# Optimization experiments

Measured on AMD Instinct MI355X. Metric: run time of the kernel, lower is better.

## Reference

```python
import jax, jax.numpy as jnp
import numpy as np

N = 100000
E = 3200000
F_IN, F_HID, F_OUT = 512, 16, 40


def setup_inputs() -> dict:
    key = jax.random.key(0)
    k1, k2, k3, k4 = jax.random.split(key, 4)
    x = jax.random.normal(k1, (N, F_IN), dtype=jnp.float32)
    edge_index = jax.random.randint(k2, (2, E), 0, N, dtype=jnp.int64)
    # Glorot-style init for the two GCN layer weights + zero biases
    W1 = jax.random.normal(k3, (F_IN, F_HID), dtype=jnp.float32) / np.sqrt(F_IN)
    b1 = jnp.zeros((F_HID,), dtype=jnp.float32)
    W2 = jax.random.normal(k4, (F_HID, F_OUT), dtype=jnp.float32) / np.sqrt(F_HID)
    b2 = jnp.zeros((F_OUT,), dtype=jnp.float32)
    return {"x": x, "edge_index": edge_index, "W1": W1, "b1": b1, "W2": W2, "b2": b2}


def _gcn_conv(x, src, dst, W, b):
    # x' = D^{-1/2} (A + I) D^{-1/2} (x W) + b   (standard GCNConv with self-loops)
    n = x.shape[0]
    h = x @ W  # [N, F_out] -- transform first (cheap edge traffic)
    deg = jax.ops.segment_sum(jnp.ones_like(dst, dtype=h.dtype), dst, num_segments=n) + 1.0  # +1 self-loop
    dinv = jax.lax.rsqrt(deg)
    msgs = h[src] * (dinv[src] * dinv[dst])[:, None]  # [E, F_out]
    agg = jax.ops.segment_sum(msgs, dst, num_segments=n)
    agg = agg + h * (dinv * dinv)[:, None]  # self-loop contribution
    return agg + b


def reference(x, edge_index, W1, b1, W2, b2):
    src, dst = edge_index[0], edge_index[1]
    h = _gcn_conv(x, src, dst, W1, b1)
    h = jax.nn.relu(h)
    # dropout is identity in eval mode (training=False)
    h = _gcn_conv(h, src, dst, W2, b2)
    return jax.nn.log_softmax(h, axis=1)
```

## Files before the change

### kernel.cpp

```cpp
#include <hip/hip_runtime.h>
#include <hip/hip_fp16.h>
#include <math.h>

#define FIN 512
#define FH 16
#define FOUT 40
#define RANGE 128
#define RSH 7
#define NB_MAX 1024
#define SRC_BITS 17
#define SRC_MASK 0x1FFFF
#define BCHUNK 4096
#define HCHUNK 16384
#define AP 17
#define GCHUNK 4096

__global__ __launch_bounds__(256) void histA_k(const int* __restrict__ dst, int E, int NB,
                                               unsigned* __restrict__ bcnt) {
  __shared__ unsigned h[NB_MAX];
  for (int b = threadIdx.x; b < NB; b += 256) h[b] = 0;
  __syncthreads();
  const int base = blockIdx.x * HCHUNK;
  const int cn = min(HCHUNK, E - base);
  for (int u = threadIdx.x; u < cn; u += 256)
    atomicAdd(&h[((unsigned)dst[base + u]) >> RSH], 1u);
  __syncthreads();
  for (int b = threadIdx.x; b < NB; b += 256) {
    unsigned c = h[b];
    if (c) atomicAdd(&bcnt[b], c);
  }
}

__global__ __launch_bounds__(1024) void scanB_k(const unsigned* __restrict__ bcnt, int NB,
                                                unsigned* __restrict__ boff,
                                                unsigned* __restrict__ bcur) {
  __shared__ unsigned ws[16];
  const int t = threadIdx.x, lane = t & 63, wid = t >> 6;
  unsigned v = (t < NB) ? bcnt[t] : 0;
  unsigned incl = v;
#pragma unroll
  for (int d = 1; d < 64; d <<= 1) {
    unsigned o = __shfl_up(incl, d);
    if (lane >= d) incl += o;
  }
  if (lane == 63) ws[wid] = incl;
  __syncthreads();
  unsigned woff = 0, tot = 0;
#pragma unroll
  for (int w = 0; w < 16; ++w) {
    unsigned s = ws[w];
    if (w < wid) woff += s;
    tot += s;
  }
  unsigned ex = woff + incl - v;
  if (t < NB) { boff[t] = ex; bcur[t] = ex; }
  if (t == 0) boff[NB] = tot;
}

__global__ __launch_bounds__(256) void bin_k(const int* __restrict__ src,
                                             const int* __restrict__ dst, int E, int NB,
                                             unsigned* __restrict__ bcur,
                                             unsigned* __restrict__ bins) {
  __shared__ unsigned hist[NB_MAX];
  __shared__ unsigned excl[NB_MAX];
  __shared__ unsigned gbase[NB_MAX];
  __shared__ unsigned lcur[NB_MAX];
  __shared__ unsigned stage[BCHUNK];
  __shared__ unsigned short sbkt[BCHUNK];
  __shared__ unsigned wtot[4];
  const int t = threadIdx.x, lane = t & 63, wid = t >> 6;
  for (int b = t; b < NB; b += 256) hist[b] = 0;
  __syncthreads();
  const int base = blockIdx.x * BCHUNK;
  const int cn = min(BCHUNK, E - base);
  for (int u = t; u < cn; u += 256)
    atomicAdd(&hist[((unsigned)dst[base + u]) >> RSH], 1u);
  __syncthreads();
  unsigned loc[4], s = 0;
#pragma unroll
  for (int j = 0; j < 4; ++j) {
    int idx = t * 4 + j;
    loc[j] = s;
    s += (idx < NB) ? hist[idx] : 0;
  }
  unsigned incl = s;
#pragma unroll
  for (int d = 1; d < 64; d <<= 1) {
    unsigned o = __shfl_up(incl, d);
    if (lane >= d) incl += o;
  }
  if (lane == 63) wtot[wid] = incl;
  __syncthreads();
  unsigned woff = 0;
  for (int w = 0; w < wid; ++w) woff += wtot[w];
  unsigned tex = woff + incl - s;
#pragma unroll
  for (int j = 0; j < 4; ++j) {
    int idx = t * 4 + j;
    if (idx < NB) excl[idx] = tex + loc[j];
  }
  __syncthreads();
  for (int b = t; b < NB; b += 256) {
    unsigned c = hist[b];
    gbase[b] = c ? atomicAdd(&bcur[b], c) : 0u;
    lcur[b] = excl[b];
  }
  __syncthreads();
  for (int u = t; u < cn; u += 256) {
    int e = base + u;
    unsigned d = (unsigned)dst[e];
    unsigned bkt = d >> RSH;
    unsigned pk = ((unsigned)src[e]) | ((d & (RANGE - 1)) << SRC_BITS);
    unsigned lr = atomicAdd(&lcur[bkt], 1u);
    stage[lr] = pk;
    sbkt[lr] = (unsigned short)bkt;
  }
  __syncthreads();
  for (int u = t; u < cn; u += 256) {
    unsigned bkt = sbkt[u];
    bins[gbase[bkt] + (u - excl[bkt])] = stage[u];
  }
}

__global__ __launch_bounds__(256) void deg_k(const unsigned* __restrict__ boff,
                                             const unsigned* __restrict__ bins, int n,
                                             float* __restrict__ dinv) {
  __shared__ unsigned dh[RANGE];
  const int t = threadIdx.x, b = blockIdx.x;
  if (t < RANGE) dh[t] = 0;
  __syncthreads();
  const unsigned jb = boff[b], je = boff[b + 1];
  for (unsigned j = jb + t; j < je; j += 256) atomicAdd(&dh[bins[j] >> SRC_BITS], 1u);
  __syncthreads();
  const int i = b * RANGE + t;
  if (t < RANGE && i < n) dinv[i] = rsqrtf((float)dh[t] + 1.0f);
}

__global__ __launch_bounds__(256) void gemm1_k(const float* __restrict__ x,
                                               const float* __restrict__ W1,
                                               const float* __restrict__ dinv, int n,
                                               __half* __restrict__ hs1) {
  __shared__ float w1s[FIN * FH];
  for (int idx = threadIdx.x; idx < FIN * FH; idx += 256) w1s[idx] = W1[idx];
  __syncthreads();

  const int row_raw = blockIdx.x * 256 + threadIdx.x;
  const int row = row_raw < n ? row_raw : n - 1;
  const float4* __restrict__ xr = (const float4*)(x + (size_t)row * FIN);

  float4 a0 = {0, 0, 0, 0}, a1 = {0, 0, 0, 0}, a2 = {0, 0, 0, 0}, a3 = {0, 0, 0, 0};

#pragma unroll 2
  for (int it = 0; it < FIN / 4; ++it) {
    float4 xv = xr[it];
    const float* wf = w1s + it * 4 * FH;
#pragma unroll
    for (int j = 0; j < 4; ++j) {
      const float xj = (j == 0) ? xv.x : (j == 1) ? xv.y : (j == 2) ? xv.z : xv.w;
      const float* wj = wf + j * FH;
      float4 w0 = *(const float4*)(wj + 0);
      float4 w1 = *(const float4*)(wj + 4);
      float4 w2 = *(const float4*)(wj + 8);
      float4 w3 = *(const float4*)(wj + 12);
      a0.x += xj * w0.x; a0.y += xj * w0.y; a0.z += xj * w0.z; a0.w += xj * w0.w;
      a1.x += xj * w1.x; a1.y += xj * w1.y; a1.z += xj * w1.z; a1.w += xj * w1.w;
      a2.x += xj * w2.x; a2.y += xj * w2.y; a2.z += xj * w2.z; a2.w += xj * w2.w;
      a3.x += xj * w3.x; a3.y += xj * w3.y; a3.z += xj * w3.z; a3.w += xj * w3.w;
    }
  }

  if (row_raw < n) {
    const float di = dinv[row];
    __half2 hb[8];
    hb[0] = __floats2half2_rn(a0.x * di, a0.y * di);
    hb[1] = __floats2half2_rn(a0.z * di, a0.w * di);
    hb[2] = __floats2half2_rn(a1.x * di, a1.y * di);
    hb[3] = __floats2half2_rn(a1.z * di, a1.w * di);
    hb[4] = __floats2half2_rn(a2.x * di, a2.y * di);
    hb[5] = __floats2half2_rn(a2.z * di, a2.w * di);
    hb[6] = __floats2half2_rn(a3.x * di, a3.y * di);
    hb[7] = __floats2half2_rn(a3.z * di, a3.w * di);
    uint4* o = (uint4*)(hs1 + (size_t)row * FH);
    o[0] = ((const uint4*)hb)[0];
    o[1] = ((const uint4*)hb)[1];
  }
}

__device__ __forceinline__ void accum_row(float* __restrict__ arow, uint4 q0, uint4 q1) {
  float2 f;
  f = __half22float2(*(const __half2*)&q0.x); atomicAdd(arow + 0, f.x);  atomicAdd(arow + 1, f.y);
  f = __half22float2(*(const __half2*)&q0.y); atomicAdd(arow + 2, f.x);  atomicAdd(arow + 3, f.y);
  f = __half22float2(*(const __half2*)&q0.z); atomicAdd(arow + 4, f.x);  atomicAdd(arow + 5, f.y);
  f = __half22float2(*(const __half2*)&q0.w); atomicAdd(arow + 6, f.x);  atomicAdd(arow + 7, f.y);
  f = __half22float2(*(const __half2*)&q1.x); atomicAdd(arow + 8, f.x);  atomicAdd(arow + 9, f.y);
  f = __half22float2(*(const __half2*)&q1.y); atomicAdd(arow + 10, f.x); atomicAdd(arow + 11, f.y);
  f = __half22float2(*(const __half2*)&q1.z); atomicAdd(arow + 12, f.x); atomicAdd(arow + 13, f.y);
  f = __half22float2(*(const __half2*)&q1.w); atomicAdd(arow + 14, f.x); atomicAdd(arow + 15, f.y);
}

__device__ __forceinline__ void edge_phase(const __half* __restrict__ tab,
                                           const unsigned* __restrict__ bins,
                                           unsigned jb, unsigned je, int t,
                                           float* __restrict__ acc) {
  for (unsigned cb = jb; cb < je; cb += GCHUNK) {
    const unsigned j0 = cb + t;
    unsigned pk[8];
    bool val[8];
#pragma unroll
    for (int i = 0; i < 8; ++i) {
      const unsigned j = j0 + i * 512;
      val[i] = (j < je);
      pk[i] = val[i] ? bins[j] : 0u;
    }
    uint4 q0[8], q1[8];
#pragma unroll
    for (int i = 0; i < 8; ++i) {
      const uint4* rp = (const uint4*)(tab + (size_t)(pk[i] & SRC_MASK) * FH);
      q0[i] = rp[0];
      q1[i] = rp[1];
    }
#pragma unroll
    for (int i = 0; i < 8; ++i) {
      if (val[i]) accum_row(acc + (pk[i] >> SRC_BITS) * AP, q0[i], q1[i]);
    }
  }
}

__global__ __launch_bounds__(512, 4) void gather1_k(const __half* __restrict__ hs1,
                                                    const unsigned* __restrict__ boff,
                                                    const unsigned* __restrict__ bins,
                                                    const float* __restrict__ dinv,
                                                    const float* __restrict__ b1, int n,
                                                    __half* __restrict__ rs) {
  __shared__ float acc[RANGE * AP];
  __shared__ float b1s[FH];
  const int t = threadIdx.x, b = blockIdx.x;
  if (t < FH) b1s[t] = b1[t];
  for (int u = t; u < RANGE * AP; u += 512) acc[u] = 0.f;
  __syncthreads();
  const unsigned jb = boff[b], je = boff[b + 1];
  edge_phase(hs1, bins, jb, je, t, acc);
  __syncthreads();
  const int base = b * RANGE;
  {
    const int node = t >> 2, sub = t & 3;
    const int i = base + node;
    if (i < n) {
      const float* arow = acc + node * AP + sub * 4;
      const float a0 = arow[0], a1 = arow[1], a2 = arow[2], a3 = arow[3];
      const __half2* hp = (const __half2*)(hs1 + (size_t)i * FH + sub * 4);
      const float2 h0 = __half22float2(hp[0]);
      const float2 h1 = __half22float2(hp[1]);
      const float d = dinv[i];
      float r0 = (a0 + h0.x) * d + b1s[sub * 4 + 0];
      float r1 = (a1 + h0.y) * d + b1s[sub * 4 + 1];
      float r2 = (a2 + h1.x) * d + b1s[sub * 4 + 2];
      float r3 = (a3 + h1.y) * d + b1s[sub * 4 + 3];
      r0 = fmaxf(r0, 0.f) * d;
      r1 = fmaxf(r1, 0.f) * d;
      r2 = fmaxf(r2, 0.f) * d;
      r3 = fmaxf(r3, 0.f) * d;
      __half2* rp = (__half2*)(rs + (size_t)i * FH + sub * 4);
      rp[0] = __floats2half2_rn(r0, r1);
      rp[1] = __floats2half2_rn(r2, r3);
    }
  }
}

__global__ __launch_bounds__(512, 4) void gather2_k(const __half* __restrict__ rs,
                                                    const unsigned* __restrict__ boff,
                                                    const unsigned* __restrict__ bins,
                                                    const float* __restrict__ dinv,
                                                    const float* __restrict__ W2,
                                                    const float* __restrict__ b2, int n,
                                                    float* __restrict__ out) {
  __shared__ float acc[RANGE * AP];
  __shared__ float w2s[FH * FOUT + FOUT];
  const int t = threadIdx.x, b = blockIdx.x;
  for (int idx = t; idx < FH * FOUT + FOUT; idx += 512)
    w2s[idx] = (idx < FH * FOUT) ? W2[idx] : b2[idx - FH * FOUT];
  for (int u = t; u < RANGE * AP; u += 512) acc[u] = 0.f;
  __syncthreads();
  const unsigned jb = boff[b], je = boff[b + 1];
  edge_phase(rs, bins, jb, je, t, acc);
  __syncthreads();
  const int base = b * RANGE;
  {
    const int node = t >> 2, sub = t & 3;
    const int i = base + node;
    if (i < n) {
      float* arow = acc + node * AP + sub * 4;
      const __half2* rp = (const __half2*)(rs + (size_t)i * FH + sub * 4);
      const float2 r0 = __half22float2(rp[0]);
      const float2 r1 = __half22float2(rp[1]);
      const float d = dinv[i];
      arow[0] = (arow[0] + r0.x) * d;
      arow[1] = (arow[1] + r0.y) * d;
      arow[2] = (arow[2] + r1.x) * d;
      arow[3] = (arow[3] + r1.y) * d;
    }
  }
  __syncthreads();
  const int lane = t & 63, wv = t >> 6;
  for (int nd = wv; nd < RANGE; nd += 8) {
    const int i = base + nd;
    if (i >= n) continue;
    float hv = (lane < FOUT) ? w2s[FH * FOUT + lane] : 0.f;
#pragma unroll
    for (int kk = 0; kk < 16; ++kk) {
      const float a = acc[nd * AP + kk];
      if (lane < FOUT) hv += a * w2s[kk * FOUT + lane];
    }
    float m = (lane < FOUT) ? hv : -INFINITY;
#pragma unroll
    for (int d = 1; d < 64; d <<= 1) m = fmaxf(m, __shfl_xor(m, d));
    float ex = (lane < FOUT) ? expf(hv - m) : 0.f;
#pragma unroll
    for (int d = 1; d < 64; d <<= 1) ex += __shfl_xor(ex, d);
    if (lane < FOUT) out[(size_t)i * FOUT + lane] = hv - m - logf(ex);
  }
}

extern "C" void kernel_launch(void* const* d_in, const int* in_sizes, int n_in,
                              void* d_out, int out_size, void* d_ws, size_t ws_size,
                              hipStream_t stream) {
  const float* x  = (const float*)d_in[0];
  const int*   ei = (const int*)d_in[1];
  const float* W1 = (const float*)d_in[2];
  const float* b1 = (const float*)d_in[3];
  const float* W2 = (const float*)d_in[4];
  const float* b2 = (const float*)d_in[5];
  float* out = (float*)d_out;

  const int n = in_sizes[0] / FIN;
  const int E = in_sizes[1] / 2;
  const int* src = ei;
  const int* dst = ei + E;
  const int NB = (n + RANGE - 1) >> RSH;

  char* ws = (char*)d_ws;
  size_t o = 0;
  auto alloc = [&](size_t bytes) {
    void* p = ws + o;
    o = (o + bytes + 255) & ~(size_t)255;
    return p;
  };
  unsigned* bcnt = (unsigned*)alloc((size_t)(NB + 1) * 4);
  unsigned* boff = (unsigned*)alloc((size_t)(NB + 1) * 4);
  unsigned* bcur = (unsigned*)alloc((size_t)NB * 4);
  float*    dinv = (float*)alloc((size_t)n * 4);
  unsigned* bins = (unsigned*)alloc((size_t)E * 4);
  __half*   hs1  = (__half*)alloc((size_t)n * FH * 2);
  __half*   rsb  = (__half*)alloc((size_t)n * FH * 2);

  hipMemsetAsync(bcnt, 0, (size_t)(NB + 1) * 4, stream);

  histA_k<<<(E + HCHUNK - 1) / HCHUNK, 256, 0, stream>>>(dst, E, NB, bcnt);
  scanB_k<<<1, 1024, 0, stream>>>(bcnt, NB, boff, bcur);
  bin_k<<<(E + BCHUNK - 1) / BCHUNK, 256, 0, stream>>>(src, dst, E, NB, bcur, bins);
  deg_k<<<NB, 256, 0, stream>>>(boff, bins, n, dinv);

  gemm1_k<<<(n + 255) / 256, 256, 0, stream>>>(x, W1, dinv, n, hs1);
  gather1_k<<<NB, 512, 0, stream>>>(hs1, boff, bins, dinv, b1, n, rsb);
  gather2_k<<<NB, 512, 0, stream>>>(rsb, boff, bins, dinv, W2, b2, n, out);
}
```

Measured before the change: 879.4 us.

## Stage gathered feature rows into LDS via direct global-to-LDS loads per wave

Rewrites the edge gather so each wave fetches neighbor feature rows straight into a per-wave LDS staging buffer using global_load_lds with 16-byte transfers. Two lanes now share each edge, each handling half of the 16-wide row, and each wave works through 128 edges per iteration. This replaces the old scheme where one thread per edge held 8 rows in registers, aiming to cut register pressure and issue gathers more efficiently. In exchange it adds 32KB of LDS per block, waits for all loads with a full vmcnt(0) barrier every iteration with no double buffering, and drops the occupancy hint from the launch bounds.

```diff
diff --git a/kernel.cpp b/kernel.cpp
--- a/kernel.cpp
+++ b/kernel.cpp
@@ -13,7 +13,14 @@
 #define BCHUNK 4096
 #define HCHUNK 16384
 #define AP 17
-#define GCHUNK 4096
+#define WED 128
+
+typedef unsigned int u32;
+
+__device__ __forceinline__ void gload_lds16(const void* g, void* l) {
+  __builtin_amdgcn_global_load_lds((const __attribute__((address_space(1))) u32*)g,
+                                   (__attribute__((address_space(3))) u32*)l, 16, 0, 0);
+}
 
 __global__ __launch_bounds__(256) void histA_k(const int* __restrict__ dst, int E, int NB,
                                                unsigned* __restrict__ bcnt) {
@@ -186,60 +193,56 @@
   }
 }
 
-__device__ __forceinline__ void accum_row(float* __restrict__ arow, uint4 q0, uint4 q1) {
-  float2 f;
-  f = __half22float2(*(const __half2*)&q0.x); atomicAdd(arow + 0, f.x);  atomicAdd(arow + 1, f.y);
-  f = __half22float2(*(const __half2*)&q0.y); atomicAdd(arow + 2, f.x);  atomicAdd(arow + 3, f.y);
-  f = __half22float2(*(const __half2*)&q0.z); atomicAdd(arow + 4, f.x);  atomicAdd(arow + 5, f.y);
-  f = __half22float2(*(const __half2*)&q0.w); atomicAdd(arow + 6, f.x);  atomicAdd(arow + 7, f.y);
-  f = __half22float2(*(const __half2*)&q1.x); atomicAdd(arow + 8, f.x);  atomicAdd(arow + 9, f.y);
-  f = __half22float2(*(const __half2*)&q1.y); atomicAdd(arow + 10, f.x); atomicAdd(arow + 11, f.y);
-  f = __half22float2(*(const __half2*)&q1.z); atomicAdd(arow + 12, f.x); atomicAdd(arow + 13, f.y);
-  f = __half22float2(*(const __half2*)&q1.w); atomicAdd(arow + 14, f.x); atomicAdd(arow + 15, f.y);
-}
-
 __device__ __forceinline__ void edge_phase(const __half* __restrict__ tab,
                                            const unsigned* __restrict__ bins,
                                            unsigned jb, unsigned je, int t,
+                                           __half* __restrict__ stage,
                                            float* __restrict__ acc) {
-  for (unsigned cb = jb; cb < je; cb += GCHUNK) {
-    const unsigned j0 = cb + t;
-    unsigned pk[8];
-    bool val[8];
-#pragma unroll
-    for (int i = 0; i < 8; ++i) {
-      const unsigned j = j0 + i * 512;
-      val[i] = (j < je);
-      pk[i] = val[i] ? bins[j] : 0u;
-    }
-    uint4 q0[8], q1[8];
-#pragma unroll
-    for (int i = 0; i < 8; ++i) {
-      const uint4* rp = (const uint4*)(tab + (size_t)(pk[i] & SRC_MASK) * FH);
-      q0[i] = rp[0];
-      q1[i] = rp[1];
-    }
-#pragma unroll
-    for (int i = 0; i < 8; ++i) {
-      if (val[i]) accum_row(acc + (pk[i] >> SRC_BITS) * AP, q0[i], q1[i]);
-    }
-  }
-}
-
-__global__ __launch_bounds__(512, 4) void gather1_k(const __half* __restrict__ hs1,
-                                                    const unsigned* __restrict__ boff,
-                                                    const unsigned* __restrict__ bins,
-                                                    const float* __restrict__ dinv,
-                                                    const float* __restrict__ b1, int n,
-                                                    __half* __restrict__ rs) {
+  const int l = t & 63, wv = t >> 6;
+  __half* swv = stage + wv * (WED * FH);
+  for (unsigned c = jb + (unsigned)wv * WED; c < je; c += 8u * WED) {
+    unsigned pk[4];
+    bool vld[4];
+#pragma unroll
+    for (int r = 0; r < 4; ++r) {
+      const unsigned e = c + r * 32u + (unsigned)(l >> 1);
+      vld[r] = (e < je);
+      pk[r] = bins[vld[r] ? e : (je - 1)];
+      const unsigned row = vld[r] ? (pk[r] & SRC_MASK) : 0u;
+      const __half* g = tab + (size_t)row * FH + (l & 1) * 8;
+      gload_lds16(g, swv + r * 512 + l * 8);
+    }
+    asm volatile("s_waitcnt vmcnt(0)" ::: "memory");
+    __builtin_amdgcn_sched_barrier(0);
+#pragma unroll
+    for (int r = 0; r < 4; ++r) {
+      if (!vld[r]) continue;
+      const uint4 q = *(const uint4*)(swv + r * 512 + l * 8);
+      float* arow = acc + (pk[r] >> SRC_BITS) * AP + (l & 1) * 8;
+      float2 f;
+      f = __half22float2(*(const __half2*)&q.x); atomicAdd(arow + 0, f.x); atomicAdd(arow + 1, f.y);
+      f = __half22float2(*(const __half2*)&q.y); atomicAdd(arow + 2, f.x); atomicAdd(arow + 3, f.y);
+      f = __half22float2(*(const __half2*)&q.z); atomicAdd(arow + 4, f.x); atomicAdd(arow + 5, f.y);
+      f = __half22float2(*(const __half2*)&q.w); atomicAdd(arow + 6, f.x); atomicAdd(arow + 7, f.y);
+    }
+  }
+}
+
+__global__ __launch_bounds__(512) void gather1_k(const __half* __restrict__ hs1,
+                                                 const unsigned* __restrict__ boff,
+                                                 const unsigned* __restrict__ bins,
+                                                 const float* __restrict__ dinv,
+                                                 const float* __restrict__ b1, int n,
+                                                 __half* __restrict__ rs) {
   __shared__ float acc[RANGE * AP];
+  __shared__ __half stage[8 * WED * FH];
   __shared__ float b1s[FH];
   const int t = threadIdx.x, b = blockIdx.x;
   if (t < FH) b1s[t] = b1[t];
   for (int u = t; u < RANGE * AP; u += 512) acc[u] = 0.f;
   __syncthreads();
   const unsigned jb = boff[b], je = boff[b + 1];
-  edge_phase(hs1, bins, jb, je, t, acc);
+  edge_phase(hs1, bins, jb, je, t, stage, acc);
   __syncthreads();
   const int base = b * RANGE;
   {
@@ -267,14 +270,15 @@
   }
 }
 
-__global__ __launch_bounds__(512, 4) void gather2_k(const __half* __restrict__ rs,
-                                                    const unsigned* __restrict__ boff,
-                                                    const unsigned* __restrict__ bins,
-                                                    const float* __restrict__ dinv,
-                                                    const float* __restrict__ W2,
-                                                    const float* __restrict__ b2, int n,
-                                                    float* __restrict__ out) {
+__global__ __launch_bounds__(512) void gather2_k(const __half* __restrict__ rs,
+                                                 const unsigned* __restrict__ boff,
+                                                 const unsigned* __restrict__ bins,
+                                                 const float* __restrict__ dinv,
+                                                 const float* __restrict__ W2,
+                                                 const float* __restrict__ b2, int n,
+                                                 float* __restrict__ out) {
   __shared__ float acc[RANGE * AP];
+  __shared__ __half stage[8 * WED * FH];
   __shared__ float w2s[FH * FOUT + FOUT];
   const int t = threadIdx.x, b = blockIdx.x;
   for (int idx = t; idx < FH * FOUT + FOUT; idx += 512)
@@ -282,7 +286,7 @@
   for (int u = t; u < RANGE * AP; u += 512) acc[u] = 0.f;
   __syncthreads();
   const unsigned jb = boff[b], je = boff[b + 1];
-  edge_phase(rs, bins, jb, je, t, acc);
+  edge_phase(rs, bins, jb, je, t, stage, acc);
   __syncthreads();
   const int base = b * RANGE;
   {
```

Result: no change. 868.6 us (-1.2%).

## Tile gather by source-row blocks staged in LDS with double-buffered async loads

Applied to the files above, without the earlier changes.

Destination buckets grow from 128 to 448 nodes. A second binning pass sorts each bucket's edges into 512-row source tiles. The gather kernels stream each source tile of the feature table into LDS through double-buffered global_load_lds and read rows from LDS rather than making random global reads. The aim is to replace scattered global gathers with coalesced tile loads, at the cost of loading every source tile for every destination block (about 196×224 tiles per layer) plus an extra binning kernel and workspace.

```diff
diff --git a/kernel.cpp b/kernel.cpp
--- a/kernel.cpp
+++ b/kernel.cpp
@@ -5,15 +5,22 @@
 #define FIN 512
 #define FH 16
 #define FOUT 40
-#define RANGE 128
-#define RSH 7
-#define NB_MAX 1024
+#define DT 448
+#define SUB 512
 #define SRC_BITS 17
 #define SRC_MASK 0x1FFFF
 #define BCHUNK 4096
 #define HCHUNK 16384
+#define NB_MAX 1024
 #define AP 17
-#define GCHUNK 4096
+#define NTS_MAX 200
+
+typedef unsigned int u32;
+
+__device__ __forceinline__ void gload_lds16(const void* g, void* l) {
+  __builtin_amdgcn_global_load_lds((const __attribute__((address_space(1))) u32*)g,
+                                   (__attribute__((address_space(3))) u32*)l, 16, 0, 0);
+}
 
 __global__ __launch_bounds__(256) void histA_k(const int* __restrict__ dst, int E, int NB,
                                                unsigned* __restrict__ bcnt) {
@@ -23,7 +30,7 @@
   const int base = blockIdx.x * HCHUNK;
   const int cn = min(HCHUNK, E - base);
   for (int u = threadIdx.x; u < cn; u += 256)
-    atomicAdd(&h[((unsigned)dst[base + u]) >> RSH], 1u);
+    atomicAdd(&h[((unsigned)dst[base + u]) / DT], 1u);
   __syncthreads();
   for (int b = threadIdx.x; b < NB; b += 256) {
     unsigned c = h[b];
@@ -74,7 +81,7 @@
   const int base = blockIdx.x * BCHUNK;
   const int cn = min(BCHUNK, E - base);
   for (int u = t; u < cn; u += 256)
-    atomicAdd(&hist[((unsigned)dst[base + u]) >> RSH], 1u);
+    atomicAdd(&hist[((unsigned)dst[base + u]) / DT], 1u);
   __syncthreads();
   unsigned loc[4], s = 0;
 #pragma unroll
@@ -109,8 +116,9 @@
   for (int u = t; u < cn; u += 256) {
     int e = base + u;
     unsigned d = (unsigned)dst[e];
-    unsigned bkt = d >> RSH;
-    unsigned pk = ((unsigned)src[e]) | ((d & (RANGE - 1)) << SRC_BITS);
+    unsigned bkt = d / DT;
+    unsigned dloc = d - bkt * DT;
+    unsigned pk = ((unsigned)src[e]) | (dloc << SRC_BITS);
     unsigned lr = atomicAdd(&lcur[bkt], 1u);
     stage[lr] = pk;
     sbkt[lr] = (unsigned short)bkt;
@@ -122,18 +130,50 @@
   }
 }
 
-__global__ __launch_bounds__(256) void deg_k(const unsigned* __restrict__ boff,
+__global__ __launch_bounds__(512) void deg_k(const unsigned* __restrict__ boff,
                                              const unsigned* __restrict__ bins, int n,
                                              float* __restrict__ dinv) {
-  __shared__ unsigned dh[RANGE];
+  __shared__ unsigned dh[DT];
   const int t = threadIdx.x, b = blockIdx.x;
-  if (t < RANGE) dh[t] = 0;
+  if (t < DT) dh[t] = 0;
   __syncthreads();
   const unsigned jb = boff[b], je = boff[b + 1];
-  for (unsigned j = jb + t; j < je; j += 256) atomicAdd(&dh[bins[j] >> SRC_BITS], 1u);
-  __syncthreads();
-  const int i = b * RANGE + t;
-  if (t < RANGE && i < n) dinv[i] = rsqrtf((float)dh[t] + 1.0f);
+  for (unsigned j = jb + t; j < je; j += 512) atomicAdd(&dh[bins[j] >> SRC_BITS], 1u);
+  __syncthreads();
+  const int i = b * DT + t;
+  if (t < DT && i < n) dinv[i] = rsqrtf((float)dh[t] + 1.0f);
+}
+
+__global__ __launch_bounds__(1024) void bin2_k(const unsigned* __restrict__ boff,
+                                               const unsigned* __restrict__ bins, int nts,
+                                               unsigned* __restrict__ out2,
+                                               unsigned* __restrict__ off2) {
+  __shared__ unsigned h2[NTS_MAX];
+  __shared__ unsigned o2[NTS_MAX + 1];
+  __shared__ unsigned cur2[NTS_MAX];
+  const int t = threadIdx.x, b = blockIdx.x;
+  const unsigned jb = boff[b], je = boff[b + 1];
+  if (t < nts) h2[t] = 0;
+  __syncthreads();
+  for (unsigned j = jb + t; j < je; j += 1024)
+    atomicAdd(&h2[(bins[j] & SRC_MASK) >> 9], 1u);
+  __syncthreads();
+  if (t == 0) {
+    unsigned s = 0;
+    for (int i = 0; i < nts; ++i) { o2[i] = s; s += h2[i]; }
+    o2[nts] = s;
+  }
+  __syncthreads();
+  if (t < nts) cur2[t] = o2[t];
+  if (t <= nts) off2[(size_t)b * (nts + 1) + t] = o2[t];
+  __syncthreads();
+  for (unsigned j = jb + t; j < je; j += 1024) {
+    const unsigned pk = bins[j];
+    const unsigned srcf = pk & SRC_MASK;
+    const unsigned st = srcf >> 9;
+    const unsigned p = atomicAdd(&cur2[st], 1u);
+    out2[jb + p] = (srcf & 511u) | ((pk >> SRC_BITS) << 9);
+  }
 }
 
 __global__ __launch_bounds__(256) void gemm1_k(const float* __restrict__ x,
@@ -143,13 +183,10 @@
   __shared__ float w1s[FIN * FH];
   for (int idx = threadIdx.x; idx < FIN * FH; idx += 256) w1s[idx] = W1[idx];
   __syncthreads();
-
   const int row_raw = blockIdx.x * 256 + threadIdx.x;
   const int row = row_raw < n ? row_raw : n - 1;
   const float4* __restrict__ xr = (const float4*)(x + (size_t)row * FIN);
-
   float4 a0 = {0, 0, 0, 0}, a1 = {0, 0, 0, 0}, a2 = {0, 0, 0, 0}, a3 = {0, 0, 0, 0};
-
 #pragma unroll 2
   for (int it = 0; it < FIN / 4; ++it) {
     float4 xv = xr[it];
@@ -168,7 +205,6 @@
       a3.x += xj * w3.x; a3.y += xj * w3.y; a3.z += xj * w3.z; a3.w += xj * w3.w;
     }
   }
-
   if (row_raw < n) {
     const float di = dinv[row];
     __half2 hb[8];
@@ -198,52 +234,68 @@
   f = __half22float2(*(const __half2*)&q1.w); atomicAdd(arow + 14, f.x); atomicAdd(arow + 15, f.y);
 }
 
-__device__ __forceinline__ void edge_phase(const __half* __restrict__ tab,
-                                           const unsigned* __restrict__ bins,
-                                           unsigned jb, unsigned je, int t,
-                                           float* __restrict__ acc) {
-  for (unsigned cb = jb; cb < je; cb += GCHUNK) {
-    const unsigned j0 = cb + t;
-    unsigned pk[8];
-    bool val[8];
-#pragma unroll
-    for (int i = 0; i < 8; ++i) {
-      const unsigned j = j0 + i * 512;
-      val[i] = (j < je);
-      pk[i] = val[i] ? bins[j] : 0u;
-    }
-    uint4 q0[8], q1[8];
-#pragma unroll
-    for (int i = 0; i < 8; ++i) {
-      const uint4* rp = (const uint4*)(tab + (size_t)(pk[i] & SRC_MASK) * FH);
-      q0[i] = rp[0];
-      q1[i] = rp[1];
-    }
-#pragma unroll
-    for (int i = 0; i < 8; ++i) {
-      if (val[i]) accum_row(acc + (pk[i] >> SRC_BITS) * AP, q0[i], q1[i]);
-    }
-  }
-}
-
-__global__ __launch_bounds__(512, 4) void gather1_k(const __half* __restrict__ hs1,
-                                                    const unsigned* __restrict__ boff,
-                                                    const unsigned* __restrict__ bins,
-                                                    const float* __restrict__ dinv,
-                                                    const float* __restrict__ b1, int n,
-                                                    __half* __restrict__ rs) {
-  __shared__ float acc[RANGE * AP];
+__device__ __forceinline__ void stage_sub(const __half* __restrict__ tab, int st,
+                                          __half* __restrict__ buf, int t) {
+  const __half* g = tab + ((size_t)st * SUB + (t >> 1)) * FH + (t & 1) * 8;
+  gload_lds16(g, buf + t * 8);
+}
+
+__device__ __forceinline__ void consume_sub(const unsigned* __restrict__ out2, unsigned jb,
+                                            unsigned a, unsigned e,
+                                            const __half* __restrict__ buf,
+                                            float* __restrict__ acc, int t) {
+  for (unsigned j = a + t; j < e; j += 1024) {
+    const unsigned pk = out2[jb + j];
+    const int srcl = pk & 511, dstl = pk >> 9;
+    const uint4 q0 = *(const uint4*)(buf + srcl * FH);
+    const uint4 q1 = *(const uint4*)(buf + srcl * FH + 8);
+    accum_row(acc + dstl * AP, q0, q1);
+  }
+}
+
+__device__ __forceinline__ void tile_gather(const __half* __restrict__ tab,
+                                            const unsigned* __restrict__ out2,
+                                            const unsigned* __restrict__ off2r,
+                                            unsigned jb, int nts, int t,
+                                            __half* __restrict__ sb0,
+                                            __half* __restrict__ sb1,
+                                            float* __restrict__ acc) {
+  for (int u = t; u < DT * AP; u += 1024) acc[u] = 0.f;
+  stage_sub(tab, 0, sb0, t);
+  __syncthreads();
+  for (int st = 0; st < nts; ++st) {
+    asm volatile("s_waitcnt vmcnt(0)" ::: "memory");
+    __builtin_amdgcn_sched_barrier(0);
+    __builtin_amdgcn_s_barrier();
+    __builtin_amdgcn_sched_barrier(0);
+    __half* cur = (st & 1) ? sb1 : sb0;
+    __half* nxt = (st & 1) ? sb0 : sb1;
+    if (st + 1 < nts) stage_sub(tab, st + 1, nxt, t);
+    consume_sub(out2, jb, off2r[st], off2r[st + 1], cur, acc, t);
+    __builtin_amdgcn_sched_barrier(0);
+    __builtin_amdgcn_s_barrier();
+    __builtin_amdgcn_sched_barrier(0);
+  }
+  __syncthreads();
+}
+
+__global__ __launch_bounds__(1024) void gath1_k(const __half* __restrict__ hs1,
+                                                const unsigned* __restrict__ boff,
+                                                const unsigned* __restrict__ out2,
+                                                const unsigned* __restrict__ off2, int nts,
+                                                const float* __restrict__ dinv,
+                                                const float* __restrict__ b1, int n,
+                                                __half* __restrict__ rs) {
+  __shared__ float acc[DT * AP];
+  __shared__ __half sb0[SUB * FH];
+  __shared__ __half sb1[SUB * FH];
   __shared__ float b1s[FH];
   const int t = threadIdx.x, b = blockIdx.x;
   if (t < FH) b1s[t] = b1[t];
-  for (int u = t; u < RANGE * AP; u += 512) acc[u] = 0.f;
-  __syncthreads();
-  const unsigned jb = boff[b], je = boff[b + 1];
-  edge_phase(hs1, bins, jb, je, t, acc);
-  __syncthreads();
-  const int base = b * RANGE;
-  {
-    const int node = t >> 2, sub = t & 3;
+  tile_gather(hs1, out2, off2 + (size_t)b * (nts + 1), boff[b], nts, t, sb0, sb1, acc);
+  const int base = b * DT;
+  for (int idx = t; idx < DT * 4; idx += 1024) {
+    const int node = idx >> 2, sub = idx & 3;
     const int i = base + node;
     if (i < n) {
       const float* arow = acc + node * AP + sub * 4;
@@ -267,26 +319,22 @@
   }
 }
 
-__global__ __launch_bounds__(512, 4) void gather2_k(const __half* __restrict__ rs,
-                                                    const unsigned* __restrict__ boff,
-                                                    const unsigned* __restrict__ bins,
-                                                    const float* __restrict__ dinv,
-                                                    const float* __restrict__ W2,
-                                                    const float* __restrict__ b2, int n,
-                                                    float* __restrict__ out) {
-  __shared__ float acc[RANGE * AP];
-  __shared__ float w2s[FH * FOUT + FOUT];
+__global__ __launch_bounds__(1024) void gath2_k(const __half* __restrict__ rs,
+                                                const unsigned* __restrict__ boff,
+                                                const unsigned* __restrict__ out2,
+                                                const unsigned* __restrict__ off2, int nts,
+                                                const float* __restrict__ dinv,
+                                                const float* __restrict__ W2,
+                                                const float* __restrict__ b2, int n,
+                                                float* __restrict__ out) {
+  __shared__ float acc[DT * AP];
+  __shared__ __half sb0[SUB * FH];
+  __shared__ __half sb1[SUB * FH];
   const int t = threadIdx.x, b = blockIdx.x;
-  for (int idx = t; idx < FH * FOUT + FOUT; idx += 512)
-    w2s[idx] = (idx < FH * FOUT) ? W2[idx] : b2[idx - FH * FOUT];
-  for (int u = t; u < RANGE * AP; u += 512) acc[u] = 0.f;
-  __syncthreads();
-  const unsigned jb = boff[b], je = boff[b + 1];
-  edge_phase(rs, bins, jb, je, t, acc);
-  __syncthreads();
-  const int base = b * RANGE;
-  {
-    const int node = t >> 2, sub = t & 3;
+  tile_gather(rs, out2, off2 + (size_t)b * (nts + 1), boff[b], nts, t, sb0, sb1, acc);
+  const int base = b * DT;
+  for (int idx = t; idx < DT * 4; idx += 1024) {
+    const int node = idx >> 2, sub = idx & 3;
     const int i = base + node;
     if (i < n) {
       float* arow = acc + node * AP + sub * 4;
@@ -301,8 +349,12 @@
     }
   }
   __syncthreads();
+  float* w2s = (float*)sb0;
+  for (int idx = t; idx < FH * FOUT + FOUT; idx += 1024)
+    w2s[idx] = (idx < FH * FOUT) ? W2[idx] : b2[idx - FH * FOUT];
+  __syncthreads();
   const int lane = t & 63, wv = t >> 6;
-  for (int nd = wv; nd < RANGE; nd += 8) {
+  for (int nd = wv; nd < DT; nd += 16) {
     const int i = base + nd;
     if (i >= n) continue;
     float hv = (lane < FOUT) ? w2s[FH * FOUT + lane] : 0.f;
@@ -336,7 +388,9 @@
   const int E = in_sizes[1] / 2;
   const int* src = ei;
   const int* dst = ei + E;
-  const int NB = (n + RANGE - 1) >> RSH;
+  const int NB  = (n + DT - 1) / DT;
+  const int NTS = (n + SUB - 1) / SUB;
+  const size_t padRows = (size_t)NTS * SUB;
 
   char* ws = (char*)d_ws;
   size_t o = 0;
@@ -350,17 +404,20 @@
   unsigned* bcur = (unsigned*)alloc((size_t)NB * 4);
   float*    dinv = (float*)alloc((size_t)n * 4);
   unsigned* bins = (unsigned*)alloc((size_t)E * 4);
-  __half*   hs1  = (__half*)alloc((size_t)n * FH * 2);
-  __half*   rsb  = (__half*)alloc((size_t)n * FH * 2);
+  unsigned* out2 = (unsigned*)alloc((size_t)E * 4);
+  unsigned* off2 = (unsigned*)alloc((size_t)NB * (NTS + 1) * 4);
+  __half*   hs1  = (__half*)alloc(padRows * FH * 2);
+  __half*   rsb  = (__half*)alloc(padRows * FH * 2);
 
   hipMemsetAsync(bcnt, 0, (size_t)(NB + 1) * 4, stream);
 
   histA_k<<<(E + HCHUNK - 1) / HCHUNK, 256, 0, stream>>>(dst, E, NB, bcnt);
   scanB_k<<<1, 1024, 0, stream>>>(bcnt, NB, boff, bcur);
   bin_k<<<(E + BCHUNK - 1) / BCHUNK, 256, 0, stream>>>(src, dst, E, NB, bcur, bins);
-  deg_k<<<NB, 256, 0, stream>>>(boff, bins, n, dinv);
+  deg_k<<<NB, 512, 0, stream>>>(boff, bins, n, dinv);
+  bin2_k<<<NB, 1024, 0, stream>>>(boff, bins, NTS, out2, off2);
 
   gemm1_k<<<(n + 255) / 256, 256, 0, stream>>>(x, W1, dinv, n, hs1);
-  gather1_k<<<NB, 512, 0, stream>>>(hs1, boff, bins, dinv, b1, n, rsb);
-  gather2_k<<<NB, 512, 0, stream>>>(rsb, boff, bins, dinv, W2, b2, n, out);
-}
+  gath1_k<<<NB, 1024, 0, stream>>>(hs1, boff, out2, off2, NTS, dinv, b1, n, rsb);
+  gath2_k<<<NB, 1024, 0, stream>>>(rsb, boff, out2, off2, NTS, dinv, W2, b2, n, out);
+}
```

Result: slower. 909.4 us (+3.4%).
